# Performance work log

Hardware: AMD Instinct MI355X
Metric: run time of the kernel (lower is better)

## Reference

```python
import jax, jax.numpy as jnp
import numpy as np

# Quantization / crossbar-simulation hyperparameters (from args)
WLA = 8          # wl_activate / wl_input bits
WLW = 8          # wl_weight bits
CELLBIT = 2      # bits stored per memory cell
ADC = 6          # ADC precision bits
SUB = 128        # crossbar subArray rows
ONOFF = 10.0     # cell on/off conductance ratio
STRIDE = 2
EPS = 1e-5


def _ste_round(v):
    return v + jax.lax.stop_gradient(jnp.round(v) - v)


def setup_inputs() -> dict:
    key = jax.random.key(0)
    ks = jax.random.split(key, 7)
    B, C, H, W, O = 16, 512, 28, 28, 1024
    x = jax.random.normal(ks[0], (B, C, H, W), dtype=jnp.float32)
    y = jax.random.normal(ks[1], (B, O, H // STRIDE, W // STRIDE), dtype=jnp.float32)
    bn_gamma = 1.0 + 0.1 * jax.random.normal(ks[2], (C,), dtype=jnp.float32)
    bn_beta = 0.1 * jax.random.normal(ks[3], (C,), dtype=jnp.float32)
    bn_mean = 0.1 * jax.random.normal(ks[4], (C,), dtype=jnp.float32)
    bn_var = jax.random.uniform(ks[5], (C,), dtype=jnp.float32, minval=0.5, maxval=1.5)
    w = 0.05 * jax.random.normal(ks[6], (O, C, 1, 1), dtype=jnp.float32)
    return {"x": x, "y": y, "bn_gamma": bn_gamma, "bn_beta": bn_beta,
            "bn_mean": bn_mean, "bn_var": bn_var, "w": w}


def _shortcut_q(x, y, bn_gamma, bn_beta, bn_mean, bn_var, w):
    # BatchNorm (inference, running stats) + ReLU
    inv = jax.lax.rsqrt(bn_var + EPS)
    xh = jax.nn.relu((x - bn_mean[None, :, None, None]) * (inv * bn_gamma)[None, :, None, None]
                     + bn_beta[None, :, None, None])

    aQ = float(2 ** WLA - 1)
    wQ = float(2 ** (WLW - 1) - 1)
    SHIFT = 2 ** (WLW - 1)  # map signed int weights to unsigned cells

    # Activation quantization to WLA unsigned bits (post-ReLU, per-tensor scale)
    a_max = jnp.maximum(jnp.max(xh), 1e-8)
    x_int = _ste_round(jnp.clip(xh / a_max, 0.0, 1.0) * aQ)          # [B,C,H,W] in [0, 255]
    xs = x_int[:, :, ::STRIDE, ::STRIDE]                              # 1x1 conv, stride 2

    # Weight quantization to WLW signed bits (per-tensor scale)
    w2 = w[:, :, 0, 0]                                                # [O,C]
    w_max = jnp.maximum(jnp.max(jnp.abs(w2)), 1e-8)
    w_int = _ste_round(jnp.clip(w2 / w_max, -1.0, 1.0) * wQ)          # [-127, 127]

    # Ideal integer conv (used for STE backward path)
    ideal = jnp.einsum('oc,bchw->bohw', w_int, xs)

    # --- analog crossbar simulation: bit-sliced inputs x cell-sliced weights + ADC ---
    cellRange = 2 ** CELLBIT
    nsl = WLW // CELLBIT
    off = (cellRange - 1) / (ONOFF - 1.0)                             # min-conductance offset
    B, C, Ho, Wo = xs.shape
    O = w2.shape[0]
    G = C // SUB                                                      # subarray groups along rows
    xg = xs.reshape(B, G, SUB, Ho, Wo)
    wu = (w_int + float(SHIFT)).reshape(O, G, SUB)                    # unsigned cell values
    vmax = SUB * (cellRange - 1 + off)                                # max per-column analog sum
    delta = vmax / float(2 ** ADC - 1)                                # ADC LSB

    sim = jnp.zeros_like(ideal)
    for z in range(WLA):                                              # input bit planes
        xb = jnp.floor(xg / (2.0 ** z)) % 2.0                         # [B,G,S,Ho,Wo] in {0,1}
        xsum = xb.sum(axis=2)                                         # dummy-column input [B,G,Ho,Wo]
        for k in range(nsl):                                          # weight cell slices
            wk = jnp.floor(wu / float(cellRange ** k)) % cellRange + off   # [O,G,S]
            dk = float((SHIFT // cellRange ** k) % cellRange) + off        # dummy cell value
            psum = jnp.einsum('ogs,bgshw->bgohw', wk, xb)             # analog column sums
            psum_q = jnp.round(psum / delta) * delta                  # ADC quantization
            dummy_q = jnp.round(dk * xsum / delta) * delta            # ADC on dummy column
            sim = sim + (2.0 ** z) * (float(cellRange) ** k) * (psum_q - dummy_q[:, :, None]).sum(axis=1)

    # STE: forward = simulated, backward = ideal quantized conv
    out_int = ideal + jax.lax.stop_gradient(sim - ideal)
    return out_int * (w_max / wQ) * (a_max / aQ) + y


def reference(x, y, bn_gamma, bn_beta, bn_mean, bn_var, w):
    return _shortcut_q(x, y, bn_gamma, bn_beta, bn_mean, bn_var, w)
```

## Files before the change

kernel.cpp:

```cpp
#include <hip/hip_runtime.h>
#include <math.h>

typedef __attribute__((ext_vector_type(4))) int i32x4;
typedef __attribute__((ext_vector_type(16))) int i32x16;

namespace {
constexpr int N_ = 3136;
constexpr int M_ = N_ * 8;
constexpr size_t FIN_OFF   = 0;
constexpr size_t AMAXP_OFF = 256;
constexpr size_t WMAXP_OFF = 4096;
constexpr size_t CHS_OFF   = 6144;
constexpr size_t DUM_OFF   = 8192;
constexpr size_t ACT_OFF   = 36864;
constexpr size_t WGT_OFF   = ACT_OFF + (size_t)M_ * 512;
}

__device__ __forceinline__ void gload(const char* g, char* l) {
  __builtin_amdgcn_global_load_lds(
      (const __attribute__((address_space(1))) char*)g,
      (__attribute__((address_space(3))) char*)l, 16, 0, 0);
}

__global__ __launch_bounds__(256) void prep1_kernel(
    const float* __restrict__ x, const float* __restrict__ w,
    const float* __restrict__ gamma, const float* __restrict__ beta,
    const float* __restrict__ mean, const float* __restrict__ var,
    float* __restrict__ amaxp, float* __restrict__ wmaxp, float* __restrict__ chs) {
#pragma clang fp contract(off)
  __shared__ float red[4];
  const int bx = blockIdx.x, tid = threadIdx.x;
  if (bx < 896) {
    int id = bx * 256 + tid;
    int row = id / 28;
    int seg = id - row * 28;
    int c = row & 511;
    const float4* p = (const float4*)(x + (size_t)row * 784 + seg * 28);
    float mn = 1e30f, mx = -1e30f;
#pragma unroll
    for (int i = 0; i < 7; ++i) {
      float4 v = p[i];
      mn = fminf(mn, fminf(fminf(v.x, v.y), fminf(v.z, v.w)));
      mx = fmaxf(mx, fmaxf(fmaxf(v.x, v.y), fmaxf(v.z, v.w)));
    }
    float vf = var[c] + 1e-5f;
    float sc = (float)(1.0 / sqrt((double)vf)) * gamma[c];
    float f1 = (mn - mean[c]) * sc + beta[c];
    float f2 = (mx - mean[c]) * sc + beta[c];
    float m = fmaxf(fmaxf(f1, f2), 0.f);
#pragma unroll
    for (int o = 32; o > 0; o >>= 1) m = fmaxf(m, __shfl_down(m, o, 64));
    if ((tid & 63) == 0) red[tid >> 6] = m;
    __syncthreads();
    if (tid == 0) amaxp[bx] = fmaxf(fmaxf(red[0], red[1]), fmaxf(red[2], red[3]));
  } else if (bx < 1152) {
    int id = (bx - 896) * 256 + tid;
    const float4* p = (const float4*)w + (size_t)id * 2;
    float4 v0 = p[0], v1 = p[1];
    float m = fmaxf(fmaxf(fmaxf(fabsf(v0.x), fabsf(v0.y)), fmaxf(fabsf(v0.z), fabsf(v0.w))),
                    fmaxf(fmaxf(fabsf(v1.x), fabsf(v1.y)), fmaxf(fabsf(v1.z), fabsf(v1.w))));
#pragma unroll
    for (int o = 32; o > 0; o >>= 1) m = fmaxf(m, __shfl_down(m, o, 64));
    if ((tid & 63) == 0) red[tid >> 6] = m;
    __syncthreads();
    if (tid == 0) wmaxp[bx - 896] = fmaxf(fmaxf(red[0], red[1]), fmaxf(red[2], red[3]));
  } else {
    int c = (bx - 1152) * 256 + tid;
    float vf = var[c] + 1e-5f;
    chs[c] = (float)(1.0 / sqrt((double)vf)) * gamma[c];
  }
}

__global__ __launch_bounds__(256) void pack_xw_kernel(
    const float* __restrict__ x, const float* __restrict__ mean,
    const float* __restrict__ beta, const float* __restrict__ chs,
    const float* __restrict__ amaxp, const float* __restrict__ w,
    const float* __restrict__ wmaxp, unsigned* __restrict__ act,
    unsigned* __restrict__ wgt, int* __restrict__ dummy_part,
    float* __restrict__ fin) {
#pragma clang fp contract(off)
  const int bx = blockIdx.x, tid = threadIdx.x;
  if (bx < 224) {
    __shared__ float samax;
    __shared__ __align__(16) unsigned char sx[28 * 256];
    __shared__ int dd[448];
    const int chalf = bx & 1;
    const int bp = (bx >> 1) % 7;
    const int b = (bx >> 1) / 7;
    if (tid < 64) {
      float m = 0.f;
      for (int i = tid; i < 896; i += 64) m = fmaxf(m, amaxp[i]);
#pragma unroll
      for (int o = 32; o > 0; o >>= 1) m = fmaxf(m, __shfl_down(m, o, 64));
      if (tid == 0) {
        float a = fmaxf(m, 1e-8f);
        samax = a;
        if (bx == 0) fin[0] = a;
      }
    }
    __syncthreads();
    const float amax = samax;
    for (int it = 0; it < 14; ++it) {
      int id = it * 256 + tid;
      int cl = id / 14, r = id - cl * 14;
      int rowsel = r / 7, f4i = r - rowsel * 7;
      int c = chalf * 256 + cl;
      const float4 v = *(const float4*)(
          x + (size_t)(b * 512 + c) * 784 + (bp * 4 + 2 * rowsel) * 28 + f4i * 4);
      float sc = chs[c], mu = mean[c], be = beta[c];
      float f0 = fmaxf((v.x - mu) * sc + be, 0.f);
      int i0 = (int)rintf(fminf(fmaxf(f0 / amax, 0.f), 1.f) * 255.0f);
      float f2 = fmaxf((v.z - mu) * sc + be, 0.f);
      int i2 = (int)rintf(fminf(fmaxf(f2 / amax, 0.f), 1.f) * 255.0f);
      int nl = rowsel * 14 + f4i * 2;
      sx[nl * 256 + cl] = (unsigned char)i0;
      sx[(nl + 1) * 256 + cl] = (unsigned char)i2;
    }
    __syncthreads();
    const int tile0 = (b * 196 + 28 * bp) >> 2;
    for (int it = 0; it < 14; ++it) {
      int id = it * 256 + tid;
      int row = id & 31, kh = (id >> 5) & 1, gjl = (id >> 6) & 7, tilel = id >> 9;
      int nl = tilel * 4 + (row >> 3), z = row & 7;
      int cl0 = (gjl >> 2) * 128 + (gjl & 3) * 32 + kh * 16;
      const uint4 v = *(const uint4*)(sx + nl * 256 + cl0);
      uint4 o;
      o.x = (v.x >> z) & 0x01010101u;
      o.y = (v.y >> z) & 0x01010101u;
      o.z = (v.z >> z) & 0x01010101u;
      o.w = (v.w >> z) & 0x01010101u;
      size_t off = (size_t)(tile0 + tilel) * 16384 +
                   (size_t)(chalf * 8 + gjl) * 1024 + kh * 512 + row * 16;
      *(uint4*)((char*)act + off) = o;
    }
    for (int it = 0; it < 2; ++it) {
      int id = it * 256 + tid;
      if (id < 448) {
        int z = id & 7, gl = (id >> 3) & 1, nl = id >> 4;
        const unsigned* sw = (const unsigned*)(sx + nl * 256 + gl * 128);
        int xs = 0;
#pragma unroll
        for (int wq = 0; wq < 8; ++wq) {
          uint4 vv = *(const uint4*)(sw + wq * 4);
          xs += __popc((vv.x >> z) & 0x01010101u) + __popc((vv.y >> z) & 0x01010101u) +
                __popc((vv.z >> z) & 0x01010101u) + __popc((vv.w >> z) & 0x01010101u);
        }
        unsigned q0 = (__umul24((unsigned)xs, 51610u) + 524288u) >> 20;
        unsigned q3 = (__umul24((unsigned)xs, 361268u) + 524288u) >> 20;
        dd[id] = (int)((__umul24(q0, 21u) + (q3 << 6)) << z);
      }
    }
    __syncthreads();
    if (tid < 28) {
      int s = 0;
#pragma unroll
      for (int i = 0; i < 16; ++i) s += dd[tid * 16 + i];
      dummy_part[(b * 196 + 28 * bp + tid) * 2 + chalf] = s;
    }
  } else {
    __shared__ float swmax;
    const int bx2 = bx - 224;
    if (tid < 64) {
      float m = fmaxf(fmaxf(wmaxp[tid], wmaxp[tid + 64]),
                      fmaxf(wmaxp[tid + 128], wmaxp[tid + 192]));
#pragma unroll
      for (int o = 32; o > 0; o >>= 1) m = fmaxf(m, __shfl_down(m, o, 64));
      if (tid == 0) {
        float a = fmaxf(m, 1e-8f);
        swmax = a;
        if (bx2 == 0) fin[1] = a;
      }
    }
    __syncthreads();
    const float wmax = swmax;
    int t = bx2 * 256 + tid;
    int c16 = t & 31, k = (t >> 5) & 3, o = t >> 7;
    unsigned words[4];
#pragma unroll
    for (int q = 0; q < 4; ++q) {
      unsigned wd = 0;
#pragma unroll
      for (int j = 0; j < 4; ++j) {
        int c = c16 * 16 + q * 4 + j;
        float v = fminf(fmaxf(w[(size_t)o * 512 + c] / wmax, -1.f), 1.f);
        int wi = (int)rintf(v * 127.0f);
        unsigned wu = (unsigned)(wi + 128);
        unsigned cell = (wu >> (2 * k)) & 3u;
        wd |= (3u * cell + 1u) << (8 * j);
      }
      words[q] = wd;
    }
    int r = o * 4 + k;
    size_t off = (size_t)(r >> 6) * 32768 + (size_t)(c16 >> 2) * 4096 +
                 (size_t)(((c16 & 3) << 6) + (r & 63)) * 16;
    *(uint4*)(wgt + (off >> 2)) = make_uint4(words[0], words[1], words[2], words[3]);
  }
}


#define APREF(off_, p_) {                                   \
  av[p_][0] = *(const i32x4*)(gA + (off_));                 \
  av[p_][1] = *(const i32x4*)(gA + (off_) + 1024);          \
  av[p_][2] = *(const i32x4*)(gA + (off_) + 2048);          \
  av[p_][3] = *(const i32x4*)(gA + (off_) + 3072);          \
}

#define GCOMP(g_, p_) {                                                       \
  i32x4 b00 = *(const i32x4*)(rB + (g_) * 8192);                              \
  i32x4 b10 = *(const i32x4*)(rB + (g_) * 8192 + 512);                        \
  i32x16 c0 = __builtin_amdgcn_mfma_i32_32x32x32_i8(av[p_][0], b00, zvec, 0, 0, 0); \
  i32x16 c1 = __builtin_amdgcn_mfma_i32_32x32x32_i8(av[p_][0], b10, zvec, 0, 0, 0); \
  _Pragma("unroll")                                                           \
  for (int j = 1; j < 4; ++j) {                                               \
    i32x4 b0 = *(const i32x4*)(rB + (g_) * 8192 + j * 2048);                  \
    i32x4 b1 = *(const i32x4*)(rB + (g_) * 8192 + j * 2048 + 512);            \
    c0 = __builtin_amdgcn_mfma_i32_32x32x32_i8(av[p_][j], b0, c0, 0, 0, 0);   \
    c1 = __builtin_amdgcn_mfma_i32_32x32x32_i8(av[p_][j], b1, c1, 0, 0, 0);   \
  }                                                                           \
  _Pragma("unroll")                                                           \
  for (int e = 0; e < 16; ++e) {                                              \
    unsigned q0q = (__umul24((unsigned)c0[e], 51610u) + 524288u) >> 20;       \
    acc[0][e >> 2] += (int)(q0q << shr[e & 3]);                               \
    unsigned q1q = (__umul24((unsigned)c1[e], 51610u) + 524288u) >> 20;       \
    acc[1][e >> 2] += (int)(q1q << shr[e & 3]);                               \
  }                                                                           \
}

#define GUNIT(i_, g_, pref_) {                                                \
  const int p_ = ((i_) * 4 + (g_)) & 1;                                       \
  if (pref_) {                                                                \
    const int nu = (i_) * 4 + (g_) + 1;                                       \
    APREF((nu >> 2) * 65536 + (nu & 3) * 4096, 1 - p_)                        \
  }                                                                           \
  GCOMP(g_, p_)                                                               \
}

#define MBLK_EPI(i_) {                                                        \
  int sums[2][4];                                                             \
  _Pragma("unroll")                                                           \
  for (int cs = 0; cs < 2; ++cs)                                              \
    _Pragma("unroll")                                                         \
    for (int cc = 0; cc < 4; ++cc) {                                          \
      int v = acc[cs][cc];                                                    \
      v += __shfl_xor(v, 1, 64);                                              \
      v += __shfl_xor(v, 2, 64);                                              \
      v += __shfl_xor(v, 32, 64);                                             \
      sums[cs][cc] = v;                                                       \
      acc[cs][cc] = 0;                                                        \
    }                                                                         \
  if ((lane & 3) == 0 && lane < 32) {                                         \
    const int ol = lane >> 2;                                                 \
    _Pragma("unroll")                                                         \
    for (int cc = 0; cc < 4; ++cc) {                                          \
      int n = (mslice * 4 + (i_)) * 16 + wm * 4 + cc;                         \
      int d = dp[n * 2] + dp[n * 2 + 1];                                      \
      int b = n / 196, hw = n - b * 196;                                      \
      _Pragma("unroll")                                                       \
      for (int cs = 0; cs < 2; ++cs) {                                        \
        int o = cblk * 16 + cs * 8 + ol;                                      \
        size_t idx = ((size_t)(b * 1024 + o)) * 196 + hw;                     \
        out[idx] = (float)(sums[cs][cc] - d) * scale + y[idx];                \
      }                                                                       \
    }                                                                         \
  }                                                                           \
}

#define MBLK(i_, last_) {                                                     \
  GUNIT(i_, 0, 1) GUNIT(i_, 1, 1) GUNIT(i_, 2, 1) GUNIT(i_, 3, !(last_))     \
  MBLK_EPI(i_)                                                                \
}

__global__ __launch_bounds__(256, 4) void shortcutq_main_kernel(
    const char* __restrict__ act, const char* __restrict__ wgt,
    const int* __restrict__ dp, const float* __restrict__ y,
    const float* __restrict__ fin, float* __restrict__ out) {
  __shared__ __align__(16) char lds[32768];
  const int tid = threadIdx.x;
  const int cblk = blockIdx.x;
  const int mslice = blockIdx.y;
  const int lane = tid & 63, wm = tid >> 6;

  const char* gA = act + (size_t)(mslice * 16 + wm) * 16384 + lane * 16;
  const char* gB = wgt + (size_t)cblk * 32768 + tid * 16;
  const char* rB = lds + (lane >> 5) * 1024 + (lane & 31) * 16;

  const int shb = 4 * (lane >> 5) + 2 * (lane & 3);
  int shr[4] = {shb, shb + 1, shb + 2, shb + 3};

  i32x4 av[2][4];
  int acc[2][4];
#pragma unroll
  for (int cs = 0; cs < 2; ++cs)
#pragma unroll
    for (int cc = 0; cc < 4; ++cc) acc[cs][cc] = 0;
  i32x16 zvec;
#pragma unroll
  for (int e = 0; e < 16; ++e) zvec[e] = 0;

  APREF(0, 0)
#pragma unroll
  for (int l = 0; l < 8; ++l)
    gload(gB + l * 4096, lds + l * 4096 + tid * 16);
  __syncthreads();

  const float scale = (float)((128.0 * (3.0 + 1.0 / 3.0)) / 63.0) *
                      (fin[1] / 127.0f) * (fin[0] / 255.0f);

  MBLK(0, 0) MBLK(1, 0) MBLK(2, 0) MBLK(3, 1)
}

extern "C" void kernel_launch(void* const* d_in, const int* in_sizes, int n_in,
                              void* d_out, int out_size, void* d_ws, size_t ws_size,
                              hipStream_t stream) {
  const float* x     = (const float*)d_in[0];
  const float* y     = (const float*)d_in[1];
  const float* gamma = (const float*)d_in[2];
  const float* beta  = (const float*)d_in[3];
  const float* mean  = (const float*)d_in[4];
  const float* var   = (const float*)d_in[5];
  const float* w     = (const float*)d_in[6];
  float* out = (float*)d_out;

  char* wsb = (char*)d_ws;
  float* fin    = (float*)(wsb + FIN_OFF);
  float* amaxp  = (float*)(wsb + AMAXP_OFF);
  float* wmaxp  = (float*)(wsb + WMAXP_OFF);
  float* chs    = (float*)(wsb + CHS_OFF);
  int*   dum    = (int*)(wsb + DUM_OFF);
  char*  actb   = wsb + ACT_OFF;
  char*  wgtb   = wsb + WGT_OFF;

  hipLaunchKernelGGL(prep1_kernel, dim3(1154), dim3(256), 0, stream,
                     x, w, gamma, beta, mean, var, amaxp, wmaxp, chs);
  hipLaunchKernelGGL(pack_xw_kernel, dim3(736), dim3(256), 0, stream,
                     x, mean, beta, chs, amaxp, w, wmaxp,
                     (unsigned*)actb, (unsigned*)wgtb, dum, fin);
  hipLaunchKernelGGL(shortcutq_main_kernel, dim3(64, 49), dim3(256), 0, stream,
                     actb, wgtb, dum, y, fin, out);
}
```

Before: 179.3 us.

## Interchange group and m-block loops to reuse LDS weight fragments across m-blocks

The unit loop is reordered so the outer loop runs over weight groups and the inner loop over the four m-blocks. Each group's B fragments are read from LDS into registers once and reused for all four m-blocks, instead of being reloaded for every m-block. Because every m-block's partial sums must now stay live until the end, the accumulators grow to four sets and all epilogues run at the end. Launch bounds drop from 4 to 3 waves per SIMD to make room for the extra registers, which costs some occupancy.

```diff
diff --git a/kernel.cpp b/kernel.cpp
--- a/kernel.cpp
+++ b/kernel.cpp
@@ -205,34 +205,39 @@
   av[p_][3] = *(const i32x4*)(gA + (off_) + 3072);          \
 }
 
-#define GCOMP(g_, p_) {                                                       \
-  i32x4 b00 = *(const i32x4*)(rB + (g_) * 8192);                              \
-  i32x4 b10 = *(const i32x4*)(rB + (g_) * 8192 + 512);                        \
-  i32x16 c0 = __builtin_amdgcn_mfma_i32_32x32x32_i8(av[p_][0], b00, zvec, 0, 0, 0); \
-  i32x16 c1 = __builtin_amdgcn_mfma_i32_32x32x32_i8(av[p_][0], b10, zvec, 0, 0, 0); \
+#define BLOADG(g_) {                                                          \
+  _Pragma("unroll")                                                           \
+  for (int j = 0; j < 4; ++j) {                                               \
+    bf[j][0] = *(const i32x4*)(rB + (g_) * 8192 + j * 2048);                  \
+    bf[j][1] = *(const i32x4*)(rB + (g_) * 8192 + j * 2048 + 512);            \
+  }                                                                           \
+}
+
+#define GCOMPN(i_, p_) {                                                      \
+  i32x16 c0 = __builtin_amdgcn_mfma_i32_32x32x32_i8(av[p_][0], bf[0][0], zvec, 0, 0, 0); \
+  i32x16 c1 = __builtin_amdgcn_mfma_i32_32x32x32_i8(av[p_][0], bf[0][1], zvec, 0, 0, 0); \
   _Pragma("unroll")                                                           \
   for (int j = 1; j < 4; ++j) {                                               \
-    i32x4 b0 = *(const i32x4*)(rB + (g_) * 8192 + j * 2048);                  \
-    i32x4 b1 = *(const i32x4*)(rB + (g_) * 8192 + j * 2048 + 512);            \
-    c0 = __builtin_amdgcn_mfma_i32_32x32x32_i8(av[p_][j], b0, c0, 0, 0, 0);   \
-    c1 = __builtin_amdgcn_mfma_i32_32x32x32_i8(av[p_][j], b1, c1, 0, 0, 0);   \
+    c0 = __builtin_amdgcn_mfma_i32_32x32x32_i8(av[p_][j], bf[j][0], c0, 0, 0, 0); \
+    c1 = __builtin_amdgcn_mfma_i32_32x32x32_i8(av[p_][j], bf[j][1], c1, 0, 0, 0); \
   }                                                                           \
   _Pragma("unroll")                                                           \
   for (int e = 0; e < 16; ++e) {                                              \
     unsigned q0q = (__umul24((unsigned)c0[e], 51610u) + 524288u) >> 20;       \
-    acc[0][e >> 2] += (int)(q0q << shr[e & 3]);                               \
+    acc[i_][0][e >> 2] += (int)(q0q << shr[e & 3]);                           \
     unsigned q1q = (__umul24((unsigned)c1[e], 51610u) + 524288u) >> 20;       \
-    acc[1][e >> 2] += (int)(q1q << shr[e & 3]);                               \
-  }                                                                           \
-}
-
-#define GUNIT(i_, g_, pref_) {                                                \
-  const int p_ = ((i_) * 4 + (g_)) & 1;                                       \
-  if (pref_) {                                                                \
-    const int nu = (i_) * 4 + (g_) + 1;                                       \
-    APREF((nu >> 2) * 65536 + (nu & 3) * 4096, 1 - p_)                        \
-  }                                                                           \
-  GCOMP(g_, p_)                                                               \
+    acc[i_][1][e >> 2] += (int)(q1q << shr[e & 3]);                           \
+  }                                                                           \
+}
+
+#define GUNIT(g_, i_) {                                                       \
+  const int u_ = (g_) * 4 + (i_);                                             \
+  const int p_ = u_ & 1;                                                      \
+  if (u_ < 15) {                                                              \
+    const int nu_ = u_ + 1;                                                   \
+    APREF((nu_ & 3) * 65536 + (nu_ >> 2) * 4096, 1 - p_)                      \
+  }                                                                           \
+  GCOMPN(i_, p_)                                                              \
 }
 
 #define MBLK_EPI(i_) {                                                        \
@@ -241,12 +246,11 @@
   for (int cs = 0; cs < 2; ++cs)                                              \
     _Pragma("unroll")                                                         \
     for (int cc = 0; cc < 4; ++cc) {                                          \
-      int v = acc[cs][cc];                                                    \
+      int v = acc[i_][cs][cc];                                                \
       v += __shfl_xor(v, 1, 64);                                              \
       v += __shfl_xor(v, 2, 64);                                              \
       v += __shfl_xor(v, 32, 64);                                             \
       sums[cs][cc] = v;                                                       \
-      acc[cs][cc] = 0;                                                        \
     }                                                                         \
   if ((lane & 3) == 0 && lane < 32) {                                         \
     const int ol = lane >> 2;                                                 \
@@ -265,12 +269,7 @@
   }                                                                           \
 }
 
-#define MBLK(i_, last_) {                                                     \
-  GUNIT(i_, 0, 1) GUNIT(i_, 1, 1) GUNIT(i_, 2, 1) GUNIT(i_, 3, !(last_))     \
-  MBLK_EPI(i_)                                                                \
-}
-
-__global__ __launch_bounds__(256, 4) void shortcutq_main_kernel(
+__global__ __launch_bounds__(256, 3) void shortcutq_main_kernel(
     const char* __restrict__ act, const char* __restrict__ wgt,
     const int* __restrict__ dp, const float* __restrict__ y,
     const float* __restrict__ fin, float* __restrict__ out) {
@@ -288,11 +287,14 @@
   int shr[4] = {shb, shb + 1, shb + 2, shb + 3};
 
   i32x4 av[2][4];
-  int acc[2][4];
-#pragma unroll
-  for (int cs = 0; cs < 2; ++cs)
-#pragma unroll
-    for (int cc = 0; cc < 4; ++cc) acc[cs][cc] = 0;
+  i32x4 bf[4][2];
+  int acc[4][2][4];
+#pragma unroll
+  for (int i = 0; i < 4; ++i)
+#pragma unroll
+    for (int cs = 0; cs < 2; ++cs)
+#pragma unroll
+      for (int cc = 0; cc < 4; ++cc) acc[i][cs][cc] = 0;
   i32x16 zvec;
 #pragma unroll
   for (int e = 0; e < 16; ++e) zvec[e] = 0;
@@ -306,7 +308,12 @@
   const float scale = (float)((128.0 * (3.0 + 1.0 / 3.0)) / 63.0) *
                       (fin[1] / 127.0f) * (fin[0] / 255.0f);
 
-  MBLK(0, 0) MBLK(1, 0) MBLK(2, 0) MBLK(3, 1)
+  BLOADG(0) GUNIT(0, 0) GUNIT(0, 1) GUNIT(0, 2) GUNIT(0, 3)
+  BLOADG(1) GUNIT(1, 0) GUNIT(1, 1) GUNIT(1, 2) GUNIT(1, 3)
+  BLOADG(2) GUNIT(2, 0) GUNIT(2, 1) GUNIT(2, 2) GUNIT(2, 3)
+  BLOADG(3) GUNIT(3, 0) GUNIT(3, 1) GUNIT(3, 2) GUNIT(3, 3)
+
+  MBLK_EPI(0) MBLK_EPI(1) MBLK_EPI(2) MBLK_EPI(3)
 }
 
 extern "C" void kernel_launch(void* const* d_in, const int* in_sizes, int n_in,
```

After: 572.8 us. +219.4%, slower.

## Fuse three kernels into one persistent kernel with grid-wide barriers

Applied to the files above, without the earlier changes.

Merges the prep, pack and main GEMM kernels into a single persistent kernel of 704 blocks that synchronises phases with an atomic grid barrier. The main phase now loops over several M-slices per block, so the weight tile loaded into LDS is reused across slices instead of being reloaded by each block. This removes two kernel launch gaps and tail effects, at the cost of requiring all 704 blocks to be co-resident, a memset before launch, and barrier spin overhead.

```diff
diff --git a/kernel.cpp b/kernel.cpp
--- a/kernel.cpp
+++ b/kernel.cpp
@@ -5,15 +5,15 @@
 typedef __attribute__((ext_vector_type(16))) int i32x16;
 
 namespace {
-constexpr int N_ = 3136;
-constexpr int M_ = N_ * 8;
+constexpr int NBLK = 704;
 constexpr size_t FIN_OFF   = 0;
+constexpr size_t BAR_OFF   = 128;
 constexpr size_t AMAXP_OFF = 256;
 constexpr size_t WMAXP_OFF = 4096;
 constexpr size_t CHS_OFF   = 6144;
 constexpr size_t DUM_OFF   = 8192;
 constexpr size_t ACT_OFF   = 36864;
-constexpr size_t WGT_OFF   = ACT_OFF + (size_t)M_ * 512;
+constexpr size_t WGT_OFF   = ACT_OFF + (size_t)25088 * 512;
 }
 
 __device__ __forceinline__ void gload(const char* g, char* l) {
@@ -22,16 +22,31 @@
       (__attribute__((address_space(3))) char*)l, 16, 0, 0);
 }
 
-__global__ __launch_bounds__(256) void prep1_kernel(
-    const float* __restrict__ x, const float* __restrict__ w,
+__device__ __forceinline__ void gridbar(unsigned* cnt, unsigned* gen) {
+  __syncthreads();
+  if (threadIdx.x == 0) {
+    __threadfence();
+    unsigned g = atomicAdd(gen, 0u);
+    if (atomicAdd(cnt, 1u) == (unsigned)NBLK - 1u) {
+      atomicExch(cnt, 0u);
+      atomicExch(gen, g + 1u);
+    } else {
+      while (atomicAdd(gen, 0u) == g) __builtin_amdgcn_s_sleep(8);
+    }
+    __threadfence();
+  }
+  __syncthreads();
+}
+
+__device__ __forceinline__ void prep_body(
+    int vb, int tid, const float* __restrict__ x, const float* __restrict__ w,
     const float* __restrict__ gamma, const float* __restrict__ beta,
     const float* __restrict__ mean, const float* __restrict__ var,
-    float* __restrict__ amaxp, float* __restrict__ wmaxp, float* __restrict__ chs) {
+    float* __restrict__ amaxp, float* __restrict__ wmaxp,
+    float* __restrict__ chs, float* red) {
 #pragma clang fp contract(off)
-  __shared__ float red[4];
-  const int bx = blockIdx.x, tid = threadIdx.x;
-  if (bx < 896) {
-    int id = bx * 256 + tid;
+  if (vb < 896) {
+    int id = vb * 256 + tid;
     int row = id / 28;
     int seg = id - row * 28;
     int c = row & 511;
@@ -52,9 +67,10 @@
     for (int o = 32; o > 0; o >>= 1) m = fmaxf(m, __shfl_down(m, o, 64));
     if ((tid & 63) == 0) red[tid >> 6] = m;
     __syncthreads();
-    if (tid == 0) amaxp[bx] = fmaxf(fmaxf(red[0], red[1]), fmaxf(red[2], red[3]));
-  } else if (bx < 1152) {
-    int id = (bx - 896) * 256 + tid;
+    if (tid == 0) amaxp[vb] = fmaxf(fmaxf(red[0], red[1]), fmaxf(red[2], red[3]));
+    __syncthreads();
+  } else if (vb < 1152) {
+    int id = (vb - 896) * 256 + tid;
     const float4* p = (const float4*)w + (size_t)id * 2;
     float4 v0 = p[0], v1 = p[1];
     float m = fmaxf(fmaxf(fmaxf(fabsf(v0.x), fabsf(v0.y)), fmaxf(fabsf(v0.z), fabsf(v0.w))),
@@ -63,140 +79,141 @@
     for (int o = 32; o > 0; o >>= 1) m = fmaxf(m, __shfl_down(m, o, 64));
     if ((tid & 63) == 0) red[tid >> 6] = m;
     __syncthreads();
-    if (tid == 0) wmaxp[bx - 896] = fmaxf(fmaxf(red[0], red[1]), fmaxf(red[2], red[3]));
-  } else {
-    int c = (bx - 1152) * 256 + tid;
+    if (tid == 0) wmaxp[vb - 896] = fmaxf(fmaxf(red[0], red[1]), fmaxf(red[2], red[3]));
+    __syncthreads();
+  } else if (vb < 1154) {
+    int c = (vb - 1152) * 256 + tid;
     float vf = var[c] + 1e-5f;
     chs[c] = (float)(1.0 / sqrt((double)vf)) * gamma[c];
   }
 }
 
-__global__ __launch_bounds__(256) void pack_xw_kernel(
-    const float* __restrict__ x, const float* __restrict__ mean,
+__device__ __forceinline__ void packx_body(
+    int vbx, int tid, const float* __restrict__ x, const float* __restrict__ mean,
     const float* __restrict__ beta, const float* __restrict__ chs,
-    const float* __restrict__ amaxp, const float* __restrict__ w,
-    const float* __restrict__ wmaxp, unsigned* __restrict__ act,
-    unsigned* __restrict__ wgt, int* __restrict__ dummy_part,
-    float* __restrict__ fin) {
+    const float* __restrict__ amaxp, unsigned* __restrict__ act,
+    int* __restrict__ dummy_part, float* __restrict__ fin, char* lds) {
 #pragma clang fp contract(off)
-  const int bx = blockIdx.x, tid = threadIdx.x;
-  if (bx < 224) {
-    __shared__ float samax;
-    __shared__ __align__(16) unsigned char sx[28 * 256];
-    __shared__ int dd[448];
-    const int chalf = bx & 1;
-    const int bp = (bx >> 1) % 7;
-    const int b = (bx >> 1) / 7;
-    if (tid < 64) {
-      float m = 0.f;
-      for (int i = tid; i < 896; i += 64) m = fmaxf(m, amaxp[i]);
-#pragma unroll
-      for (int o = 32; o > 0; o >>= 1) m = fmaxf(m, __shfl_down(m, o, 64));
-      if (tid == 0) {
-        float a = fmaxf(m, 1e-8f);
-        samax = a;
-        if (bx == 0) fin[0] = a;
+  unsigned char* sx = (unsigned char*)lds;
+  int* dd = (int*)(lds + 7168);
+  float* samax = (float*)(lds + 8960);
+  const int chalf = vbx & 1;
+  const int bp = (vbx >> 1) % 7;
+  const int b = (vbx >> 1) / 7;
+  if (tid < 64) {
+    float m = 0.f;
+    for (int i = tid; i < 896; i += 64) m = fmaxf(m, amaxp[i]);
+#pragma unroll
+    for (int o = 32; o > 0; o >>= 1) m = fmaxf(m, __shfl_down(m, o, 64));
+    if (tid == 0) {
+      float a = fmaxf(m, 1e-8f);
+      *samax = a;
+      if (vbx == 0) fin[0] = a;
+    }
+  }
+  __syncthreads();
+  const float amax = *samax;
+  for (int it = 0; it < 14; ++it) {
+    int id = it * 256 + tid;
+    int cl = id / 14, r = id - cl * 14;
+    int rowsel = r / 7, f4i = r - rowsel * 7;
+    int c = chalf * 256 + cl;
+    const float4 v = *(const float4*)(
+        x + (size_t)(b * 512 + c) * 784 + (bp * 4 + 2 * rowsel) * 28 + f4i * 4);
+    float sc = chs[c], mu = mean[c], be = beta[c];
+    float f0 = fmaxf((v.x - mu) * sc + be, 0.f);
+    int i0 = (int)rintf(fminf(fmaxf(f0 / amax, 0.f), 1.f) * 255.0f);
+    float f2 = fmaxf((v.z - mu) * sc + be, 0.f);
+    int i2 = (int)rintf(fminf(fmaxf(f2 / amax, 0.f), 1.f) * 255.0f);
+    int nl = rowsel * 14 + f4i * 2;
+    sx[nl * 256 + cl] = (unsigned char)i0;
+    sx[(nl + 1) * 256 + cl] = (unsigned char)i2;
+  }
+  __syncthreads();
+  const int tile0 = (b * 196 + 28 * bp) >> 2;
+  for (int it = 0; it < 14; ++it) {
+    int id = it * 256 + tid;
+    int row = id & 31, kh = (id >> 5) & 1, gjl = (id >> 6) & 7, tilel = id >> 9;
+    int nl = tilel * 4 + (row >> 3), z = row & 7;
+    int cl0 = (gjl >> 2) * 128 + (gjl & 3) * 32 + kh * 16;
+    const uint4 v = *(const uint4*)(sx + nl * 256 + cl0);
+    uint4 o;
+    o.x = (v.x >> z) & 0x01010101u;
+    o.y = (v.y >> z) & 0x01010101u;
+    o.z = (v.z >> z) & 0x01010101u;
+    o.w = (v.w >> z) & 0x01010101u;
+    size_t off = (size_t)(tile0 + tilel) * 16384 +
+                 (size_t)(chalf * 8 + gjl) * 1024 + kh * 512 + row * 16;
+    *(uint4*)((char*)act + off) = o;
+  }
+  for (int it = 0; it < 2; ++it) {
+    int id = it * 256 + tid;
+    if (id < 448) {
+      int z = id & 7, gl = (id >> 3) & 1, nl = id >> 4;
+      const unsigned* sw = (const unsigned*)(sx + nl * 256 + gl * 128);
+      int xs = 0;
+#pragma unroll
+      for (int wq = 0; wq < 8; ++wq) {
+        uint4 vv = *(const uint4*)(sw + wq * 4);
+        xs += __popc((vv.x >> z) & 0x01010101u) + __popc((vv.y >> z) & 0x01010101u) +
+              __popc((vv.z >> z) & 0x01010101u) + __popc((vv.w >> z) & 0x01010101u);
       }
-    }
-    __syncthreads();
-    const float amax = samax;
-    for (int it = 0; it < 14; ++it) {
-      int id = it * 256 + tid;
-      int cl = id / 14, r = id - cl * 14;
-      int rowsel = r / 7, f4i = r - rowsel * 7;
-      int c = chalf * 256 + cl;
-      const float4 v = *(const float4*)(
-          x + (size_t)(b * 512 + c) * 784 + (bp * 4 + 2 * rowsel) * 28 + f4i * 4);
-      float sc = chs[c], mu = mean[c], be = beta[c];
-      float f0 = fmaxf((v.x - mu) * sc + be, 0.f);
-      int i0 = (int)rintf(fminf(fmaxf(f0 / amax, 0.f), 1.f) * 255.0f);
-      float f2 = fmaxf((v.z - mu) * sc + be, 0.f);
-      int i2 = (int)rintf(fminf(fmaxf(f2 / amax, 0.f), 1.f) * 255.0f);
-      int nl = rowsel * 14 + f4i * 2;
-      sx[nl * 256 + cl] = (unsigned char)i0;
-      sx[(nl + 1) * 256 + cl] = (unsigned char)i2;
-    }
-    __syncthreads();
-    const int tile0 = (b * 196 + 28 * bp) >> 2;
-    for (int it = 0; it < 14; ++it) {
-      int id = it * 256 + tid;
-      int row = id & 31, kh = (id >> 5) & 1, gjl = (id >> 6) & 7, tilel = id >> 9;
-      int nl = tilel * 4 + (row >> 3), z = row & 7;
-      int cl0 = (gjl >> 2) * 128 + (gjl & 3) * 32 + kh * 16;
-      const uint4 v = *(const uint4*)(sx + nl * 256 + cl0);
-      uint4 o;
-      o.x = (v.x >> z) & 0x01010101u;
-      o.y = (v.y >> z) & 0x01010101u;
-      o.z = (v.z >> z) & 0x01010101u;
-      o.w = (v.w >> z) & 0x01010101u;
-      size_t off = (size_t)(tile0 + tilel) * 16384 +
-                   (size_t)(chalf * 8 + gjl) * 1024 + kh * 512 + row * 16;
-      *(uint4*)((char*)act + off) = o;
-    }
-    for (int it = 0; it < 2; ++it) {
-      int id = it * 256 + tid;
-      if (id < 448) {
-        int z = id & 7, gl = (id >> 3) & 1, nl = id >> 4;
-        const unsigned* sw = (const unsigned*)(sx + nl * 256 + gl * 128);
-        int xs = 0;
-#pragma unroll
-        for (int wq = 0; wq < 8; ++wq) {
-          uint4 vv = *(const uint4*)(sw + wq * 4);
-          xs += __popc((vv.x >> z) & 0x01010101u) + __popc((vv.y >> z) & 0x01010101u) +
-                __popc((vv.z >> z) & 0x01010101u) + __popc((vv.w >> z) & 0x01010101u);
-        }
-        unsigned q0 = (__umul24((unsigned)xs, 51610u) + 524288u) >> 20;
-        unsigned q3 = (__umul24((unsigned)xs, 361268u) + 524288u) >> 20;
-        dd[id] = (int)((__umul24(q0, 21u) + (q3 << 6)) << z);
-      }
-    }
-    __syncthreads();
-    if (tid < 28) {
-      int s = 0;
-#pragma unroll
-      for (int i = 0; i < 16; ++i) s += dd[tid * 16 + i];
-      dummy_part[(b * 196 + 28 * bp + tid) * 2 + chalf] = s;
-    }
-  } else {
-    __shared__ float swmax;
-    const int bx2 = bx - 224;
-    if (tid < 64) {
-      float m = fmaxf(fmaxf(wmaxp[tid], wmaxp[tid + 64]),
-                      fmaxf(wmaxp[tid + 128], wmaxp[tid + 192]));
-#pragma unroll
-      for (int o = 32; o > 0; o >>= 1) m = fmaxf(m, __shfl_down(m, o, 64));
-      if (tid == 0) {
-        float a = fmaxf(m, 1e-8f);
-        swmax = a;
-        if (bx2 == 0) fin[1] = a;
-      }
-    }
-    __syncthreads();
-    const float wmax = swmax;
-    int t = bx2 * 256 + tid;
-    int c16 = t & 31, k = (t >> 5) & 3, o = t >> 7;
-    unsigned words[4];
-#pragma unroll
-    for (int q = 0; q < 4; ++q) {
-      unsigned wd = 0;
-#pragma unroll
-      for (int j = 0; j < 4; ++j) {
-        int c = c16 * 16 + q * 4 + j;
-        float v = fminf(fmaxf(w[(size_t)o * 512 + c] / wmax, -1.f), 1.f);
-        int wi = (int)rintf(v * 127.0f);
-        unsigned wu = (unsigned)(wi + 128);
-        unsigned cell = (wu >> (2 * k)) & 3u;
-        wd |= (3u * cell + 1u) << (8 * j);
-      }
-      words[q] = wd;
-    }
-    int r = o * 4 + k;
-    size_t off = (size_t)(r >> 6) * 32768 + (size_t)(c16 >> 2) * 4096 +
-                 (size_t)(((c16 & 3) << 6) + (r & 63)) * 16;
-    *(uint4*)(wgt + (off >> 2)) = make_uint4(words[0], words[1], words[2], words[3]);
-  }
-}
-
+      unsigned q0 = (__umul24((unsigned)xs, 51610u) + 524288u) >> 20;
+      unsigned q3 = (__umul24((unsigned)xs, 361268u) + 524288u) >> 20;
+      dd[id] = (int)((__umul24(q0, 21u) + (q3 << 6)) << z);
+    }
+  }
+  __syncthreads();
+  if (tid < 28) {
+    int s = 0;
+#pragma unroll
+    for (int i = 0; i < 16; ++i) s += dd[tid * 16 + i];
+    dummy_part[(b * 196 + 28 * bp + tid) * 2 + chalf] = s;
+  }
+  __syncthreads();
+}
+
+__device__ __forceinline__ void packw_body(
+    int vb2, int tid, const float* __restrict__ w, const float* __restrict__ wmaxp,
+    unsigned* __restrict__ wgt, float* __restrict__ fin, char* lds) {
+#pragma clang fp contract(off)
+  float* swmax = (float*)(lds + 8960);
+  if (tid < 64) {
+    float m = fmaxf(fmaxf(wmaxp[tid], wmaxp[tid + 64]),
+                    fmaxf(wmaxp[tid + 128], wmaxp[tid + 192]));
+#pragma unroll
+    for (int o = 32; o > 0; o >>= 1) m = fmaxf(m, __shfl_down(m, o, 64));
+    if (tid == 0) {
+      float a = fmaxf(m, 1e-8f);
+      *swmax = a;
+      if (vb2 == 0) fin[1] = a;
+    }
+  }
+  __syncthreads();
+  const float wmax = *swmax;
+  int t = vb2 * 256 + tid;
+  int c16 = t & 31, k = (t >> 5) & 3, o = t >> 7;
+  unsigned words[4];
+#pragma unroll
+  for (int q = 0; q < 4; ++q) {
+    unsigned wd = 0;
+#pragma unroll
+    for (int j = 0; j < 4; ++j) {
+      int c = c16 * 16 + q * 4 + j;
+      float v = fminf(fmaxf(w[(size_t)o * 512 + c] / wmax, -1.f), 1.f);
+      int wi = (int)rintf(v * 127.0f);
+      unsigned wu = (unsigned)(wi + 128);
+      unsigned cell = (wu >> (2 * k)) & 3u;
+      wd |= (3u * cell + 1u) << (8 * j);
+    }
+    words[q] = wd;
+  }
+  int r = o * 4 + k;
+  size_t off = (size_t)(r >> 6) * 32768 + (size_t)(c16 >> 2) * 4096 +
+               (size_t)(((c16 & 3) << 6) + (r & 63)) * 16;
+  *(uint4*)(wgt + (off >> 2)) = make_uint4(words[0], words[1], words[2], words[3]);
+  __syncthreads();
+}
 
 #define APREF(off_, p_) {                                   \
   av[p_][0] = *(const i32x4*)(gA + (off_));                 \
@@ -252,8 +269,8 @@
     const int ol = lane >> 2;                                                 \
     _Pragma("unroll")                                                         \
     for (int cc = 0; cc < 4; ++cc) {                                          \
-      int n = (mslice * 4 + (i_)) * 16 + wm * 4 + cc;                         \
-      int d = dp[n * 2] + dp[n * 2 + 1];                                      \
+      int n = (msl * 4 + (i_)) * 16 + wm * 4 + cc;                            \
+      int d = dum[n * 2] + dum[n * 2 + 1];                                    \
       int b = n / 196, hw = n - b * 196;                                      \
       _Pragma("unroll")                                                       \
       for (int cs = 0; cs < 2; ++cs) {                                        \
@@ -270,43 +287,59 @@
   MBLK_EPI(i_)                                                                \
 }
 
-__global__ __launch_bounds__(256, 4) void shortcutq_main_kernel(
-    const char* __restrict__ act, const char* __restrict__ wgt,
-    const int* __restrict__ dp, const float* __restrict__ y,
-    const float* __restrict__ fin, float* __restrict__ out) {
+__global__ __launch_bounds__(256, 4) void shortcutq_mega_kernel(
+    const float* __restrict__ x, const float* __restrict__ y,
+    const float* __restrict__ gamma, const float* __restrict__ beta,
+    const float* __restrict__ mean, const float* __restrict__ var,
+    const float* __restrict__ w, float* __restrict__ fin,
+    float* __restrict__ amaxp, float* __restrict__ wmaxp,
+    float* __restrict__ chs, int* __restrict__ dum,
+    char* __restrict__ actb, char* __restrict__ wgtb,
+    unsigned* __restrict__ bar, float* __restrict__ out) {
   __shared__ __align__(16) char lds[32768];
-  const int tid = threadIdx.x;
-  const int cblk = blockIdx.x;
-  const int mslice = blockIdx.y;
+  const int bx = blockIdx.x, tid = threadIdx.x;
+
+  prep_body(bx, tid, x, w, gamma, beta, mean, var, amaxp, wmaxp, chs, (float*)lds);
+  prep_body(bx + 704, tid, x, w, gamma, beta, mean, var, amaxp, wmaxp, chs, (float*)lds);
+  gridbar(bar, bar + 1);
+
+  if (bx < 224) {
+    packx_body(bx, tid, x, mean, beta, chs, amaxp, (unsigned*)actb, dum, fin, lds);
+  } else if (bx < 480) {
+    packw_body((bx - 224) * 2 + 0, tid, w, wmaxp, (unsigned*)wgtb, fin, lds);
+    packw_body((bx - 224) * 2 + 1, tid, w, wmaxp, (unsigned*)wgtb, fin, lds);
+  }
+  gridbar(bar, bar + 1);
+
   const int lane = tid & 63, wm = tid >> 6;
-
-  const char* gA = act + (size_t)(mslice * 16 + wm) * 16384 + lane * 16;
-  const char* gB = wgt + (size_t)cblk * 32768 + tid * 16;
+  const int cblk = bx & 63, q = bx >> 6;
+  const char* gB = wgtb + (size_t)cblk * 32768 + tid * 16;
+#pragma unroll
+  for (int l = 0; l < 8; ++l)
+    gload(gB + l * 4096, lds + l * 4096 + tid * 16);
+  __syncthreads();
   const char* rB = lds + (lane >> 5) * 1024 + (lane & 31) * 16;
-
   const int shb = 4 * (lane >> 5) + 2 * (lane & 3);
   int shr[4] = {shb, shb + 1, shb + 2, shb + 3};
-
-  i32x4 av[2][4];
-  int acc[2][4];
-#pragma unroll
-  for (int cs = 0; cs < 2; ++cs)
-#pragma unroll
-    for (int cc = 0; cc < 4; ++cc) acc[cs][cc] = 0;
   i32x16 zvec;
 #pragma unroll
   for (int e = 0; e < 16; ++e) zvec[e] = 0;
-
-  APREF(0, 0)
-#pragma unroll
-  for (int l = 0; l < 8; ++l)
-    gload(gB + l * 4096, lds + l * 4096 + tid * 16);
-  __syncthreads();
-
   const float scale = (float)((128.0 * (3.0 + 1.0 / 3.0)) / 63.0) *
                       (fin[1] / 127.0f) * (fin[0] / 255.0f);
-
-  MBLK(0, 0) MBLK(1, 0) MBLK(2, 0) MBLK(3, 1)
+  const int nm = (q < 5) ? 5 : 4;
+#pragma unroll 1
+  for (int kjob = 0; kjob < nm; ++kjob) {
+    const int msl = q + 11 * kjob;
+    const char* gA = actb + (size_t)(msl * 16 + wm) * 16384 + lane * 16;
+    i32x4 av[2][4];
+    int acc[2][4];
+#pragma unroll
+    for (int cs = 0; cs < 2; ++cs)
+#pragma unroll
+      for (int cc = 0; cc < 4; ++cc) acc[cs][cc] = 0;
+    APREF(0, 0)
+    MBLK(0, 0) MBLK(1, 0) MBLK(2, 0) MBLK(3, 1)
+  }
 }
 
 extern "C" void kernel_launch(void* const* d_in, const int* in_sizes, int n_in,
@@ -322,19 +355,17 @@
   float* out = (float*)d_out;
 
   char* wsb = (char*)d_ws;
-  float* fin    = (float*)(wsb + FIN_OFF);
-  float* amaxp  = (float*)(wsb + AMAXP_OFF);
-  float* wmaxp  = (float*)(wsb + WMAXP_OFF);
-  float* chs    = (float*)(wsb + CHS_OFF);
-  int*   dum    = (int*)(wsb + DUM_OFF);
-  char*  actb   = wsb + ACT_OFF;
-  char*  wgtb   = wsb + WGT_OFF;
-
-  hipLaunchKernelGGL(prep1_kernel, dim3(1154), dim3(256), 0, stream,
-                     x, w, gamma, beta, mean, var, amaxp, wmaxp, chs);
-  hipLaunchKernelGGL(pack_xw_kernel, dim3(736), dim3(256), 0, stream,
-                     x, mean, beta, chs, amaxp, w, wmaxp,
-                     (unsigned*)actb, (unsigned*)wgtb, dum, fin);
-  hipLaunchKernelGGL(shortcutq_main_kernel, dim3(64, 49), dim3(256), 0, stream,
-                     actb, wgtb, dum, y, fin, out);
-}
+  float*    fin   = (float*)(wsb + FIN_OFF);
+  unsigned* bar   = (unsigned*)(wsb + BAR_OFF);
+  float*    amaxp = (float*)(wsb + AMAXP_OFF);
+  float*    wmaxp = (float*)(wsb + WMAXP_OFF);
+  float*    chs   = (float*)(wsb + CHS_OFF);
+  int*      dum   = (int*)(wsb + DUM_OFF);
+  char*     actb  = wsb + ACT_OFF;
+  char*     wgtb  = wsb + WGT_OFF;
+
+  hipMemsetAsync(bar, 0, 16, stream);
+  hipLaunchKernelGGL(shortcutq_mega_kernel, dim3(NBLK), dim3(256), 0, stream,
+                     x, y, gamma, beta, mean, var, w, fin, amaxp, wmaxp, chs,
+                     dum, actb, wgtb, bar, out);
+}
```

Result: slower. 539.4 us (+200.8%).
